# Kernel optimization log

Measured on AMD Instinct MI355X. Metric: run time of the kernel, lower is better.

## Reference

```python
import jax, jax.numpy as jnp
import numpy as np
from itertools import permutations
from math import factorial

N_MODES = 6
BATCH = 32768

# Clements mesh mode pairs for 6 modes: alternating odd/even layers, 15 MZIs total.
def clements_mode_list(n=6):
    pairs = []
    for layer in range(n):
        start = 0 if layer % 2 == 0 else 1
        for m in range(start, n - 1, 2):
            pairs.append((m, m + 1))
    return pairs

CLEMENTS_MODES = clements_mode_list(6)            # 15 pairs
ANSATZ_MODES = [(0, 1), (2, 3), (4, 5), (1, 2), (3, 4)] * 2  # 10 pairs (0-indexed)

IN_CONFIG = [1, 1, 1, 0, 0, 0]
OUT_CONFIGS = [list(c) for c in [
    [1,1,1,0,0,0],[1,1,0,1,0,0],[1,1,0,0,1,0],[1,1,0,0,0,1],[1,0,1,1,0,0],
    [1,0,1,0,1,0],[1,0,1,0,0,1],[1,0,0,1,1,0],[1,0,0,1,0,1],[1,0,0,0,1,1],
    [0,1,1,1,0,0],[0,1,1,0,1,0],[0,1,1,0,0,1],[0,1,0,1,1,0],[0,1,0,1,0,1],
    [0,1,0,0,1,1],[0,0,1,1,1,0],[0,0,1,1,0,1],[0,0,1,0,1,1],[0,0,0,1,1,1]]]

def _expand(config):  # occupation list -> repeated mode indices
    idx = []
    for m, c in enumerate(config):
        idx += [m] * int(c)
    return idx

IN_IDX = np.array(_expand(IN_CONFIG))                       # [3]
OUT_IDX = np.array([_expand(c) for c in OUT_CONFIGS])       # [20, 3]
N_PH = IN_IDX.shape[0]                                      # 3 photons
PERMS = list(permutations(range(N_PH)))                     # 6 perms of S_3
# boson-sampling normalization: sqrt(prod(in!) * prod(out!)) per output config (all 1 here)
NORM = np.array([np.sqrt(np.prod([factorial(int(v)) for v in IN_CONFIG]) *
                         np.prod([factorial(int(v)) for v in c])) for c in OUT_CONFIGS],
                dtype=np.float32)


def calc_unitary(modes, theta, phi):
    """Chain of MZI 2x2 rotations embedded in a 6x6 identity (Clements convention)."""
    U = jnp.eye(N_MODES, dtype=jnp.complex64)
    for k, (m, n) in enumerate(modes):
        ct = jnp.cos(theta[k]).astype(jnp.complex64)
        st = jnp.sin(theta[k]).astype(jnp.complex64)
        ep = jnp.exp(1j * phi[k].astype(jnp.complex64))
        T = jnp.eye(N_MODES, dtype=jnp.complex64)
        T = T.at[m, m].set(ep * ct).at[m, n].set(-st)
        T = T.at[n, m].set(ep * st).at[n, n].set(ct)
        U = T @ U
    return U


def permanent3(M):  # M: [..., 3, 3] complex -> [...] permanent over S_3
    acc = jnp.zeros(M.shape[:-2], dtype=M.dtype)
    for p in PERMS:
        acc = acc + M[..., 0, p[0]] * M[..., 1, p[1]] * M[..., 2, p[2]]
    return acc


def setup_inputs() -> dict:
    key = jax.random.key(0)
    ks = jax.random.split(key, 7)
    return {
        "x": jax.random.normal(ks[0], (BATCH, 12), dtype=jnp.float32),
        "params": jax.random.normal(ks[1], (30,), dtype=jnp.float32),
        "output_phase": jax.random.normal(ks[2], (6,), dtype=jnp.float32),
        "param_phi": jax.random.normal(ks[3], (4,), dtype=jnp.float32),
        "param_theta": jax.random.normal(ks[4], (4,), dtype=jnp.float32),
        "input_k": jax.random.normal(ks[5], (12,), dtype=jnp.float32),
        "input_b": jax.random.normal(ks[6], (12,), dtype=jnp.float32),
    }


def reference(x, params, output_phase, param_phi, param_theta, input_k, input_b):
    B = x.shape[0]
    # Static 6x6 interferometer: phi = params[0:15], theta = params[15:30]
    start = calc_unitary(CLEMENTS_MODES, params[15:30], params[0:15])
    start = jnp.diag(jnp.exp(1j * output_phase.astype(jnp.complex64))) @ start

    # Data-reuploading ansatz angles, [B, 10] each
    xs = x * input_k + input_b
    phi = jnp.concatenate([xs[:, 0:3], jnp.broadcast_to(param_phi[0:2], (B, 2)),
                           xs[:, 6:9], jnp.broadcast_to(param_phi[2:4], (B, 2))], axis=1)
    theta = jnp.concatenate([xs[:, 3:6], jnp.broadcast_to(param_theta[0:2], (B, 2)),
                             xs[:, 9:12], jnp.broadcast_to(param_theta[2:4], (B, 2))], axis=1)

    U_ans = jax.vmap(lambda t, p: calc_unitary(ANSATZ_MODES, t, p))(theta, phi)  # [B,6,6]
    U_final = U_ans @ start                                                      # [B,6,6]

    # Boson-sampling amplitudes: permanent of [out rows, in cols] submatrix
    sub = U_final[:, OUT_IDX[:, :, None], IN_IDX[None, None, :]]  # [B, 20, 3, 3]
    amps = permanent3(sub) / jnp.asarray(NORM)                    # [B, 20] complex

    # F.normalize(p=2, dim=1, eps=1e-12) on complex vectors
    norm = jnp.sqrt(jnp.sum(jnp.abs(amps) ** 2, axis=1, keepdims=True))
    amps = amps / jnp.maximum(norm, 1e-12)
    return jnp.abs(amps)
```

## Files before the change

kernel.cpp:

```cpp
#include <hip/hip_runtime.h>
#include <math.h>


__global__ __launch_bounds__(64) void bqnn_kernel(
    const float* __restrict__ x,
    const float* __restrict__ params,
    const float* __restrict__ output_phase,
    const float* __restrict__ param_phi,
    const float* __restrict__ param_theta,
    const float* __restrict__ input_k,
    const float* __restrict__ input_b,
    float* __restrict__ out,
    int B)
{
    __shared__ float sSre[6][3], sSim[6][3];
    __shared__ float sC[4][4];
    __shared__ float sK[12], sB[12];

    if (threadIdx.x == 0) {
        const int CM[15][2] = {{0,1},{2,3},{4,5},{1,2},{3,4},
                               {0,1},{2,3},{4,5},{1,2},{3,4},
                               {0,1},{2,3},{4,5},{1,2},{3,4}};
        float Vre[6][3], Vim[6][3];
        #pragma unroll
        for (int r = 0; r < 6; ++r)
            #pragma unroll
            for (int c = 0; c < 3; ++c) { Vre[r][c] = (r == c) ? 1.f : 0.f; Vim[r][c] = 0.f; }
        for (int k = 0; k < 15; ++k) {
            float ct, st, epr, epi;
            __sincosf(params[15 + k], &st, &ct);
            __sincosf(params[k],      &epi, &epr);
            int m = CM[k][0], n = CM[k][1];
            #pragma unroll
            for (int c = 0; c < 3; ++c) {
                float ar = Vre[m][c], ai = Vim[m][c];
                float br = Vre[n][c], bi = Vim[n][c];
                float tr = epr * ar - epi * ai;
                float ti = epr * ai + epi * ar;
                Vre[m][c] = ct * tr - st * br;
                Vim[m][c] = ct * ti - st * bi;
                Vre[n][c] = st * tr + ct * br;
                Vim[n][c] = st * ti + ct * bi;
            }
        }
        #pragma unroll
        for (int r = 0; r < 6; ++r) {
            float pr, pi;
            __sincosf(output_phase[r], &pi, &pr);
            #pragma unroll
            for (int c = 0; c < 3; ++c) {
                sSre[r][c] = pr * Vre[r][c] - pi * Vim[r][c];
                sSim[r][c] = pr * Vim[r][c] + pi * Vre[r][c];
            }
        }
        #pragma unroll
        for (int j = 0; j < 4; ++j) {
            float ct, st, epr, epi;
            __sincosf(param_theta[j], &st, &ct);
            __sincosf(param_phi[j],   &epi, &epr);
            sC[j][0] = ct; sC[j][1] = st; sC[j][2] = epr; sC[j][3] = epi;
        }
        #pragma unroll
        for (int i = 0; i < 12; ++i) { sK[i] = input_k[i]; sB[i] = input_b[i]; }
    }
    __syncthreads();

    int b = blockIdx.x * blockDim.x + threadIdx.x;
    if (b >= B) return;

    const float4* xp = reinterpret_cast<const float4*>(x + (size_t)b * 12);
    float4 a0 = xp[0], a1 = xp[1], a2 = xp[2];
    float xs[12] = {a0.x, a0.y, a0.z, a0.w, a1.x, a1.y, a1.z, a1.w, a2.x, a2.y, a2.z, a2.w};
    #pragma unroll
    for (int i = 0; i < 12; ++i) xs[i] = xs[i] * sK[i] + sB[i];

    float ct[10], st[10], epr[10], epi[10];
    __sincosf(xs[3],  &st[0], &ct[0]);  __sincosf(xs[0], &epi[0], &epr[0]);
    __sincosf(xs[4],  &st[1], &ct[1]);  __sincosf(xs[1], &epi[1], &epr[1]);
    __sincosf(xs[5],  &st[2], &ct[2]);  __sincosf(xs[2], &epi[2], &epr[2]);
    ct[3] = sC[0][0]; st[3] = sC[0][1]; epr[3] = sC[0][2]; epi[3] = sC[0][3];
    ct[4] = sC[1][0]; st[4] = sC[1][1]; epr[4] = sC[1][2]; epi[4] = sC[1][3];
    __sincosf(xs[9],  &st[5], &ct[5]);  __sincosf(xs[6], &epi[5], &epr[5]);
    __sincosf(xs[10], &st[6], &ct[6]);  __sincosf(xs[7], &epi[6], &epr[6]);
    __sincosf(xs[11], &st[7], &ct[7]);  __sincosf(xs[8], &epi[7], &epr[7]);
    ct[8] = sC[2][0]; st[8] = sC[2][1]; epr[8] = sC[2][2]; epi[8] = sC[2][3];
    ct[9] = sC[3][0]; st[9] = sC[3][1]; epr[9] = sC[3][2]; epi[9] = sC[3][3];

    float Vre[6][3], Vim[6][3];
    #pragma unroll
    for (int r = 0; r < 6; ++r)
        #pragma unroll
        for (int c = 0; c < 3; ++c) { Vre[r][c] = sSre[r][c]; Vim[r][c] = sSim[r][c]; }

    const int AM[10][2] = {{0,1},{2,3},{4,5},{1,2},{3,4},{0,1},{2,3},{4,5},{1,2},{3,4}};
    #pragma unroll
    for (int k = 0; k < 10; ++k) {
        int m = AM[k][0], n = AM[k][1];
        #pragma unroll
        for (int c = 0; c < 3; ++c) {
            float ar = Vre[m][c], ai = Vim[m][c];
            float br = Vre[n][c], bi = Vim[n][c];
            float tr = epr[k] * ar - epi[k] * ai;
            float ti = epr[k] * ai + epi[k] * ar;
            Vre[m][c] = ct[k] * tr - st[k] * br;
            Vim[m][c] = ct[k] * ti - st[k] * bi;
            Vre[n][c] = st[k] * tr + ct[k] * br;
            Vim[n][c] = st[k] * ti + ct[k] * bi;
        }
    }

    const int PR[10][2] = {{1,2},{1,3},{1,4},{1,5},{2,3},{2,4},{2,5},{3,4},{3,5},{4,5}};
    float q01r[10], q01i[10], q02r[10], q02i[10], q12r[10], q12i[10];
    #pragma unroll
    for (int p = 0; p < 10; ++p) {
        int i = PR[p][0], j = PR[p][1];
        q01r[p] = (Vre[i][0]*Vre[j][1] - Vim[i][0]*Vim[j][1]) + (Vre[i][1]*Vre[j][0] - Vim[i][1]*Vim[j][0]);
        q01i[p] = (Vre[i][0]*Vim[j][1] + Vim[i][0]*Vre[j][1]) + (Vre[i][1]*Vim[j][0] + Vim[i][1]*Vre[j][0]);
        q02r[p] = (Vre[i][0]*Vre[j][2] - Vim[i][0]*Vim[j][2]) + (Vre[i][2]*Vre[j][0] - Vim[i][2]*Vim[j][0]);
        q02i[p] = (Vre[i][0]*Vim[j][2] + Vim[i][0]*Vre[j][2]) + (Vre[i][2]*Vim[j][0] + Vim[i][2]*Vre[j][0]);
        q12r[p] = (Vre[i][1]*Vre[j][2] - Vim[i][1]*Vim[j][2]) + (Vre[i][2]*Vre[j][1] - Vim[i][2]*Vim[j][1]);
        q12i[p] = (Vre[i][1]*Vim[j][2] + Vim[i][1]*Vre[j][2]) + (Vre[i][2]*Vim[j][1] + Vim[i][2]*Vre[j][1]);
    }

    const int TA[20] = {0,0,0,0,0,0,0,0,0,0, 1,1,1,1,1,1, 2,2,2, 3};
    const int TP[20] = {0,1,2,3,4,5,6,7,8,9, 4,5,6,7,8,9, 7,8,9, 9};
    float sq[20];
    float ssum = 0.f;
    #pragma unroll
    for (int t = 0; t < 20; ++t) {
        int a = TA[t], p = TP[t];
        float pr = (Vre[a][0]*q12r[p] - Vim[a][0]*q12i[p])
                 + (Vre[a][1]*q02r[p] - Vim[a][1]*q02i[p])
                 + (Vre[a][2]*q01r[p] - Vim[a][2]*q01i[p]);
        float pi = (Vre[a][0]*q12i[p] + Vim[a][0]*q12r[p])
                 + (Vre[a][1]*q02i[p] + Vim[a][1]*q02r[p])
                 + (Vre[a][2]*q01i[p] + Vim[a][2]*q01r[p]);
        sq[t] = pr * pr + pi * pi;
        ssum += sq[t];
    }
    float inv = 1.f / fmaxf(sqrtf(ssum), 1e-12f);
    float res[20];
    #pragma unroll
    for (int t = 0; t < 20; ++t) res[t] = sqrtf(sq[t]) * inv;

    float4* op = reinterpret_cast<float4*>(out + (size_t)b * 20);
    op[0] = make_float4(res[0],  res[1],  res[2],  res[3]);
    op[1] = make_float4(res[4],  res[5],  res[6],  res[7]);
    op[2] = make_float4(res[8],  res[9],  res[10], res[11]);
    op[3] = make_float4(res[12], res[13], res[14], res[15]);
    op[4] = make_float4(res[16], res[17], res[18], res[19]);
}

extern "C" void kernel_launch(void* const* d_in, const int* in_sizes, int n_in,
                              void* d_out, int out_size, void* d_ws, size_t ws_size,
                              hipStream_t stream) {
    const float* x            = (const float*)d_in[0];
    const float* params       = (const float*)d_in[1];
    const float* output_phase = (const float*)d_in[2];
    const float* param_phi    = (const float*)d_in[3];
    const float* param_theta  = (const float*)d_in[4];
    const float* input_k      = (const float*)d_in[5];
    const float* input_b      = (const float*)d_in[6];
    int B = in_sizes[0] / 12;

    int block = 64;
    int grid = (B + block - 1) / block;
    bqnn_kernel<<<grid, block, 0, stream>>>(x, params, output_phase, param_phi,
                                            param_theta, input_k, input_b,
                                            (float*)d_out, B);
}
```

Baseline: 12.62 us.

## Split each batch row's permanent computation across four threads

Assigns four threads per batch element. Each thread redundantly builds the full 6x3 unitary, then computes 5 of the 20 permanents with no shared pair products. The norm is reduced across the four lanes with xor shuffles and an rsqrt. This raises parallelism and lowers per-thread register pressure, but repeats the sincos and MZI chain four times, loses the reuse of the pair products, and replaces float4 output stores with scalar stores.

```diff
diff --git a/kernel.cpp b/kernel.cpp
--- a/kernel.cpp
+++ b/kernel.cpp
@@ -2,7 +2,7 @@
 #include <math.h>
 
 
-__global__ __launch_bounds__(64) void bqnn_kernel(
+__global__ __launch_bounds__(256) void bqnn_kernel(
     const float* __restrict__ x,
     const float* __restrict__ params,
     const float* __restrict__ output_phase,
@@ -65,7 +65,9 @@
     }
     __syncthreads();
 
-    int b = blockIdx.x * blockDim.x + threadIdx.x;
+    int tid = blockIdx.x * blockDim.x + threadIdx.x;
+    int b   = tid >> 2;
+    int sub = tid & 3;
     if (b >= B) return;
 
     const float4* xp = reinterpret_cast<const float4*>(x + (size_t)b * 12);
@@ -109,46 +111,42 @@
         }
     }
 
+    const int TA[20] = {0,0,0,0,0,0,0,0,0,0, 1,1,1,1,1,1, 2,2,2, 3};
+    const int TP[20] = {0,1,2,3,4,5,6,7,8,9, 4,5,6,7,8,9, 7,8,9, 9};
     const int PR[10][2] = {{1,2},{1,3},{1,4},{1,5},{2,3},{2,4},{2,5},{3,4},{3,5},{4,5}};
-    float q01r[10], q01i[10], q02r[10], q02i[10], q12r[10], q12i[10];
+
+    float sq[5];
+    float ssum = 0.f;
     #pragma unroll
-    for (int p = 0; p < 10; ++p) {
-        int i = PR[p][0], j = PR[p][1];
-        q01r[p] = (Vre[i][0]*Vre[j][1] - Vim[i][0]*Vim[j][1]) + (Vre[i][1]*Vre[j][0] - Vim[i][1]*Vim[j][0]);
-        q01i[p] = (Vre[i][0]*Vim[j][1] + Vim[i][0]*Vre[j][1]) + (Vre[i][1]*Vim[j][0] + Vim[i][1]*Vre[j][0]);
-        q02r[p] = (Vre[i][0]*Vre[j][2] - Vim[i][0]*Vim[j][2]) + (Vre[i][2]*Vre[j][0] - Vim[i][2]*Vim[j][0]);
-        q02i[p] = (Vre[i][0]*Vim[j][2] + Vim[i][0]*Vre[j][2]) + (Vre[i][2]*Vim[j][0] + Vim[i][2]*Vre[j][0]);
-        q12r[p] = (Vre[i][1]*Vre[j][2] - Vim[i][1]*Vim[j][2]) + (Vre[i][2]*Vre[j][1] - Vim[i][2]*Vim[j][1]);
-        q12i[p] = (Vre[i][1]*Vim[j][2] + Vim[i][1]*Vre[j][2]) + (Vre[i][2]*Vim[j][1] + Vim[i][2]*Vre[j][1]);
+    for (int u = 0; u < 5; ++u) {
+        int t = 5 * sub + u;
+        int a = TA[t];
+        int i = PR[TP[t]][0], j = PR[TP[t]][1];
+
+        float q01r = (Vre[i][0]*Vre[j][1] - Vim[i][0]*Vim[j][1]) + (Vre[i][1]*Vre[j][0] - Vim[i][1]*Vim[j][0]);
+        float q01i = (Vre[i][0]*Vim[j][1] + Vim[i][0]*Vre[j][1]) + (Vre[i][1]*Vim[j][0] + Vim[i][1]*Vre[j][0]);
+        float q02r = (Vre[i][0]*Vre[j][2] - Vim[i][0]*Vim[j][2]) + (Vre[i][2]*Vre[j][0] - Vim[i][2]*Vim[j][0]);
+        float q02i = (Vre[i][0]*Vim[j][2] + Vim[i][0]*Vre[j][2]) + (Vre[i][2]*Vim[j][0] + Vim[i][2]*Vre[j][0]);
+        float q12r = (Vre[i][1]*Vre[j][2] - Vim[i][1]*Vim[j][2]) + (Vre[i][2]*Vre[j][1] - Vim[i][2]*Vim[j][1]);
+        float q12i = (Vre[i][1]*Vim[j][2] + Vim[i][1]*Vre[j][2]) + (Vre[i][2]*Vim[j][1] + Vim[i][2]*Vre[j][1]);
+
+        float pr = (Vre[a][0]*q12r - Vim[a][0]*q12i)
+                 + (Vre[a][1]*q02r - Vim[a][1]*q02i)
+                 + (Vre[a][2]*q01r - Vim[a][2]*q01i);
+        float pi = (Vre[a][0]*q12i + Vim[a][0]*q12r)
+                 + (Vre[a][1]*q02i + Vim[a][1]*q02r)
+                 + (Vre[a][2]*q01i + Vim[a][2]*q01r);
+        sq[u] = pr * pr + pi * pi;
+        ssum += sq[u];
     }
 
-    const int TA[20] = {0,0,0,0,0,0,0,0,0,0, 1,1,1,1,1,1, 2,2,2, 3};
-    const int TP[20] = {0,1,2,3,4,5,6,7,8,9, 4,5,6,7,8,9, 7,8,9, 9};
-    float sq[20];
-    float ssum = 0.f;
+    ssum += __shfl_xor(ssum, 1, 64);
+    ssum += __shfl_xor(ssum, 2, 64);
+    float inv = rsqrtf(fmaxf(ssum, 1e-24f));
+
+    float* op = out + (size_t)b * 20 + sub * 5;
     #pragma unroll
-    for (int t = 0; t < 20; ++t) {
-        int a = TA[t], p = TP[t];
-        float pr = (Vre[a][0]*q12r[p] - Vim[a][0]*q12i[p])
-                 + (Vre[a][1]*q02r[p] - Vim[a][1]*q02i[p])
-                 + (Vre[a][2]*q01r[p] - Vim[a][2]*q01i[p]);
-        float pi = (Vre[a][0]*q12i[p] + Vim[a][0]*q12r[p])
-                 + (Vre[a][1]*q02i[p] + Vim[a][1]*q02r[p])
-                 + (Vre[a][2]*q01i[p] + Vim[a][2]*q01r[p]);
-        sq[t] = pr * pr + pi * pi;
-        ssum += sq[t];
-    }
-    float inv = 1.f / fmaxf(sqrtf(ssum), 1e-12f);
-    float res[20];
-    #pragma unroll
-    for (int t = 0; t < 20; ++t) res[t] = sqrtf(sq[t]) * inv;
-
-    float4* op = reinterpret_cast<float4*>(out + (size_t)b * 20);
-    op[0] = make_float4(res[0],  res[1],  res[2],  res[3]);
-    op[1] = make_float4(res[4],  res[5],  res[6],  res[7]);
-    op[2] = make_float4(res[8],  res[9],  res[10], res[11]);
-    op[3] = make_float4(res[12], res[13], res[14], res[15]);
-    op[4] = make_float4(res[16], res[17], res[18], res[19]);
+    for (int u = 0; u < 5; ++u) op[u] = sqrtf(sq[u]) * inv;
 }
 
 extern "C" void kernel_launch(void* const* d_in, const int* in_sizes, int n_in,
@@ -163,8 +161,9 @@
     const float* input_b      = (const float*)d_in[6];
     int B = in_sizes[0] / 12;
 
-    int block = 64;
-    int grid = (B + block - 1) / block;
+    int block = 256;
+    long long threads = (long long)B * 4;
+    int grid = (int)((threads + block - 1) / block);
     bqnn_kernel<<<grid, block, 0, stream>>>(x, params, output_phase, param_phi,
                                             param_theta, input_k, input_b,
                                             (float*)d_out, B);
```

Result: slower. 20.26 us (+60.5%).

## Hoist batch-invariant unitary setup into a separate single-thread kernel

Applied to the files above, without the earlier changes.

The fixed Clements unitary, the constant ansatz rotation coefficients and the input scale/bias are now computed once by a one-thread setup kernel and written to workspace. Previously thread 0 of every block redid this work, leaving the other threads waiting at a barrier. The main kernel now reads the values straight from global memory, with no shared memory and no __syncthreads. This adds a second kernel launch and a dependency between the two kernels. The normalisation also switches to rsqrtf.

```diff
diff --git a/kernel.cpp b/kernel.cpp
--- a/kernel.cpp
+++ b/kernel.cpp
@@ -2,77 +2,91 @@
 #include <math.h>
 
 
-__global__ __launch_bounds__(64) void bqnn_kernel(
-    const float* __restrict__ x,
+__global__ void setup_kernel(
     const float* __restrict__ params,
     const float* __restrict__ output_phase,
     const float* __restrict__ param_phi,
     const float* __restrict__ param_theta,
     const float* __restrict__ input_k,
     const float* __restrict__ input_b,
+    float* __restrict__ ws)
+{
+    float pct[15], pst[15], per[15], pei[15];
+    #pragma unroll
+    for (int k = 0; k < 15; ++k) {
+        __sincosf(params[15 + k], &pst[k], &pct[k]);
+        __sincosf(params[k],      &pei[k], &per[k]);
+    }
+    const int CM[15][2] = {{0,1},{2,3},{4,5},{1,2},{3,4},
+                           {0,1},{2,3},{4,5},{1,2},{3,4},
+                           {0,1},{2,3},{4,5},{1,2},{3,4}};
+    float Vre[6][3], Vim[6][3];
+    #pragma unroll
+    for (int r = 0; r < 6; ++r)
+        #pragma unroll
+        for (int c = 0; c < 3; ++c) { Vre[r][c] = (r == c) ? 1.f : 0.f; Vim[r][c] = 0.f; }
+    #pragma unroll
+    for (int k = 0; k < 15; ++k) {
+        int m = CM[k][0], n = CM[k][1];
+        #pragma unroll
+        for (int c = 0; c < 3; ++c) {
+            float ar = Vre[m][c], ai = Vim[m][c];
+            float br = Vre[n][c], bi = Vim[n][c];
+            float tr = per[k] * ar - pei[k] * ai;
+            float ti = per[k] * ai + pei[k] * ar;
+            Vre[m][c] = pct[k] * tr - pst[k] * br;
+            Vim[m][c] = pct[k] * ti - pst[k] * bi;
+            Vre[n][c] = pst[k] * tr + pct[k] * br;
+            Vim[n][c] = pst[k] * ti + pct[k] * bi;
+        }
+    }
+    #pragma unroll
+    for (int r = 0; r < 6; ++r) {
+        float pr, pi;
+        __sincosf(output_phase[r], &pi, &pr);
+        #pragma unroll
+        for (int c = 0; c < 3; ++c) {
+            ws[r * 3 + c]      = pr * Vre[r][c] - pi * Vim[r][c];
+            ws[18 + r * 3 + c] = pr * Vim[r][c] + pi * Vre[r][c];
+        }
+    }
+    #pragma unroll
+    for (int j = 0; j < 4; ++j) {
+        float ct, st, epr, epi;
+        __sincosf(param_theta[j], &st, &ct);
+        __sincosf(param_phi[j],   &epi, &epr);
+        ws[36 + j * 4 + 0] = ct;  ws[36 + j * 4 + 1] = st;
+        ws[36 + j * 4 + 2] = epr; ws[36 + j * 4 + 3] = epi;
+    }
+    #pragma unroll
+    for (int i = 0; i < 12; ++i) { ws[52 + i] = input_k[i]; ws[64 + i] = input_b[i]; }
+}
+
+__global__ __launch_bounds__(64) void bqnn_kernel(
+    const float* __restrict__ x,
+    const float* __restrict__ ws,
     float* __restrict__ out,
     int B)
 {
-    __shared__ float sSre[6][3], sSim[6][3];
-    __shared__ float sC[4][4];
-    __shared__ float sK[12], sB[12];
-
-    if (threadIdx.x == 0) {
-        const int CM[15][2] = {{0,1},{2,3},{4,5},{1,2},{3,4},
-                               {0,1},{2,3},{4,5},{1,2},{3,4},
-                               {0,1},{2,3},{4,5},{1,2},{3,4}};
-        float Vre[6][3], Vim[6][3];
-        #pragma unroll
-        for (int r = 0; r < 6; ++r)
-            #pragma unroll
-            for (int c = 0; c < 3; ++c) { Vre[r][c] = (r == c) ? 1.f : 0.f; Vim[r][c] = 0.f; }
-        for (int k = 0; k < 15; ++k) {
-            float ct, st, epr, epi;
-            __sincosf(params[15 + k], &st, &ct);
-            __sincosf(params[k],      &epi, &epr);
-            int m = CM[k][0], n = CM[k][1];
-            #pragma unroll
-            for (int c = 0; c < 3; ++c) {
-                float ar = Vre[m][c], ai = Vim[m][c];
-                float br = Vre[n][c], bi = Vim[n][c];
-                float tr = epr * ar - epi * ai;
-                float ti = epr * ai + epi * ar;
-                Vre[m][c] = ct * tr - st * br;
-                Vim[m][c] = ct * ti - st * bi;
-                Vre[n][c] = st * tr + ct * br;
-                Vim[n][c] = st * ti + ct * bi;
-            }
-        }
-        #pragma unroll
-        for (int r = 0; r < 6; ++r) {
-            float pr, pi;
-            __sincosf(output_phase[r], &pi, &pr);
-            #pragma unroll
-            for (int c = 0; c < 3; ++c) {
-                sSre[r][c] = pr * Vre[r][c] - pi * Vim[r][c];
-                sSim[r][c] = pr * Vim[r][c] + pi * Vre[r][c];
-            }
-        }
-        #pragma unroll
-        for (int j = 0; j < 4; ++j) {
-            float ct, st, epr, epi;
-            __sincosf(param_theta[j], &st, &ct);
-            __sincosf(param_phi[j],   &epi, &epr);
-            sC[j][0] = ct; sC[j][1] = st; sC[j][2] = epr; sC[j][3] = epi;
-        }
-        #pragma unroll
-        for (int i = 0; i < 12; ++i) { sK[i] = input_k[i]; sB[i] = input_b[i]; }
-    }
-    __syncthreads();
-
     int b = blockIdx.x * blockDim.x + threadIdx.x;
     if (b >= B) return;
+
+    float Sre[6][3], Sim[6][3];
+    #pragma unroll
+    for (int r = 0; r < 6; ++r)
+        #pragma unroll
+        for (int c = 0; c < 3; ++c) { Sre[r][c] = ws[r * 3 + c]; Sim[r][c] = ws[18 + r * 3 + c]; }
+    float sC[4][4];
+    #pragma unroll
+    for (int j = 0; j < 4; ++j)
+        #pragma unroll
+        for (int q = 0; q < 4; ++q) sC[j][q] = ws[36 + j * 4 + q];
 
     const float4* xp = reinterpret_cast<const float4*>(x + (size_t)b * 12);
     float4 a0 = xp[0], a1 = xp[1], a2 = xp[2];
     float xs[12] = {a0.x, a0.y, a0.z, a0.w, a1.x, a1.y, a1.z, a1.w, a2.x, a2.y, a2.z, a2.w};
     #pragma unroll
-    for (int i = 0; i < 12; ++i) xs[i] = xs[i] * sK[i] + sB[i];
+    for (int i = 0; i < 12; ++i) xs[i] = xs[i] * ws[52 + i] + ws[64 + i];
 
     float ct[10], st[10], epr[10], epi[10];
     __sincosf(xs[3],  &st[0], &ct[0]);  __sincosf(xs[0], &epi[0], &epr[0]);
@@ -90,7 +104,7 @@
     #pragma unroll
     for (int r = 0; r < 6; ++r)
         #pragma unroll
-        for (int c = 0; c < 3; ++c) { Vre[r][c] = sSre[r][c]; Vim[r][c] = sSim[r][c]; }
+        for (int c = 0; c < 3; ++c) { Vre[r][c] = Sre[r][c]; Vim[r][c] = Sim[r][c]; }
 
     const int AM[10][2] = {{0,1},{2,3},{4,5},{1,2},{3,4},{0,1},{2,3},{4,5},{1,2},{3,4}};
     #pragma unroll
@@ -138,7 +152,7 @@
         sq[t] = pr * pr + pi * pi;
         ssum += sq[t];
     }
-    float inv = 1.f / fmaxf(sqrtf(ssum), 1e-12f);
+    float inv = rsqrtf(fmaxf(ssum, 1e-24f));
     float res[20];
     #pragma unroll
     for (int t = 0; t < 20; ++t) res[t] = sqrtf(sq[t]) * inv;
@@ -162,10 +176,12 @@
     const float* input_k      = (const float*)d_in[5];
     const float* input_b      = (const float*)d_in[6];
     int B = in_sizes[0] / 12;
+    float* ws = (float*)d_ws;
+
+    setup_kernel<<<1, 1, 0, stream>>>(params, output_phase, param_phi, param_theta,
+                                      input_k, input_b, ws);
 
     int block = 64;
     int grid = (B + block - 1) / block;
-    bqnn_kernel<<<grid, block, 0, stream>>>(x, params, output_phase, param_phi,
-                                            param_theta, input_k, input_b,
-                                            (float*)d_out, B);
+    bqnn_kernel<<<grid, block, 0, stream>>>(x, ws, (float*)d_out, B);
 }
```

After: 15.17 us. 1.2x slower.

## Process two batch elements per thread and parallelize constant-mesh setup across lanes

Applied to the files above, without the earlier changes.

Each thread now handles two batch elements (tid and tid+half), and the grid is halved. The serial thread-0 setup is replaced: 44 lanes compute the sincos values in parallel, and every thread then rebuilds the fixed 6x3 mesh product in registers, which removes the long single-lane prologue before the barrier. The q-products and permanent evaluation are fused into a single loop. The gains are more ILP per thread and a shorter serialized prologue. In exchange, register pressure goes up, and every thread redoes the mesh setup.

```diff
diff --git a/kernel.cpp b/kernel.cpp
--- a/kernel.cpp
+++ b/kernel.cpp
@@ -13,142 +13,163 @@
     float* __restrict__ out,
     int B)
 {
-    __shared__ float sSre[6][3], sSim[6][3];
-    __shared__ float sC[4][4];
-    __shared__ float sK[12], sB[12];
+    __shared__ float sc[88];
+    int lane = threadIdx.x;
+    if (lane < 44) {
+        float arg;
+        if      (lane < 15) arg = params[15 + lane];
+        else if (lane < 30) arg = params[lane - 15];
+        else if (lane < 36) arg = output_phase[lane - 30];
+        else if (lane < 40) arg = param_theta[lane - 36];
+        else                arg = param_phi[lane - 40];
+        float s, c;
+        __sincosf(arg, &s, &c);
+        sc[2 * lane]     = s;
+        sc[2 * lane + 1] = c;
+    }
+    __syncthreads();
 
-    if (threadIdx.x == 0) {
-        const int CM[15][2] = {{0,1},{2,3},{4,5},{1,2},{3,4},
-                               {0,1},{2,3},{4,5},{1,2},{3,4},
-                               {0,1},{2,3},{4,5},{1,2},{3,4}};
-        float Vre[6][3], Vim[6][3];
+    const int CM[15][2] = {{0,1},{2,3},{4,5},{1,2},{3,4},
+                           {0,1},{2,3},{4,5},{1,2},{3,4},
+                           {0,1},{2,3},{4,5},{1,2},{3,4}};
+    float Sre[6][3], Sim[6][3];
+    #pragma unroll
+    for (int r = 0; r < 6; ++r)
+        #pragma unroll
+        for (int c = 0; c < 3; ++c) { Sre[r][c] = (r == c) ? 1.f : 0.f; Sim[r][c] = 0.f; }
+    #pragma unroll
+    for (int k = 0; k < 15; ++k) {
+        float pst = sc[2 * k],        pct = sc[2 * k + 1];
+        float pei = sc[2 * (15 + k)], per = sc[2 * (15 + k) + 1];
+        int m = CM[k][0], n = CM[k][1];
+        #pragma unroll
+        for (int c = 0; c < 3; ++c) {
+            float ar = Sre[m][c], ai = Sim[m][c];
+            float br = Sre[n][c], bi = Sim[n][c];
+            float tr = per * ar - pei * ai;
+            float ti = per * ai + pei * ar;
+            Sre[m][c] = pct * tr - pst * br;
+            Sim[m][c] = pct * ti - pst * bi;
+            Sre[n][c] = pst * tr + pct * br;
+            Sim[n][c] = pst * ti + pct * bi;
+        }
+    }
+    #pragma unroll
+    for (int r = 0; r < 6; ++r) {
+        float pi = sc[2 * (30 + r)], pr = sc[2 * (30 + r) + 1];
+        #pragma unroll
+        for (int c = 0; c < 3; ++c) {
+            float vr = Sre[r][c], vi = Sim[r][c];
+            Sre[r][c] = pr * vr - pi * vi;
+            Sim[r][c] = pr * vi + pi * vr;
+        }
+    }
+
+    int half = (B + 1) >> 1;
+    int tid = blockIdx.x * blockDim.x + threadIdx.x;
+    if (tid >= half) return;
+    int e1v = tid + half;
+    bool has1 = (e1v < B);
+    int eidx[2] = { tid, has1 ? e1v : tid };
+
+    float xs[2][12];
+    #pragma unroll
+    for (int e = 0; e < 2; ++e) {
+        const float4* xp = reinterpret_cast<const float4*>(x + (size_t)eidx[e] * 12);
+        float4 a0 = xp[0], a1 = xp[1], a2 = xp[2];
+        float t[12] = {a0.x, a0.y, a0.z, a0.w, a1.x, a1.y, a1.z, a1.w, a2.x, a2.y, a2.z, a2.w};
+        #pragma unroll
+        for (int i = 0; i < 12; ++i) xs[e][i] = t[i] * input_k[i] + input_b[i];
+    }
+
+    float ct[2][10], st[2][10], epr[2][10], epi[2][10];
+    #pragma unroll
+    for (int e = 0; e < 2; ++e) {
+        __sincosf(xs[e][3],  &st[e][0], &ct[e][0]);  __sincosf(xs[e][0], &epi[e][0], &epr[e][0]);
+        __sincosf(xs[e][4],  &st[e][1], &ct[e][1]);  __sincosf(xs[e][1], &epi[e][1], &epr[e][1]);
+        __sincosf(xs[e][5],  &st[e][2], &ct[e][2]);  __sincosf(xs[e][2], &epi[e][2], &epr[e][2]);
+        st[e][3] = sc[2*36]; ct[e][3] = sc[2*36+1];  epi[e][3] = sc[2*40]; epr[e][3] = sc[2*40+1];
+        st[e][4] = sc[2*37]; ct[e][4] = sc[2*37+1];  epi[e][4] = sc[2*41]; epr[e][4] = sc[2*41+1];
+        __sincosf(xs[e][9],  &st[e][5], &ct[e][5]);  __sincosf(xs[e][6], &epi[e][5], &epr[e][5]);
+        __sincosf(xs[e][10], &st[e][6], &ct[e][6]);  __sincosf(xs[e][7], &epi[e][6], &epr[e][6]);
+        __sincosf(xs[e][11], &st[e][7], &ct[e][7]);  __sincosf(xs[e][8], &epi[e][7], &epr[e][7]);
+        st[e][8] = sc[2*38]; ct[e][8] = sc[2*38+1];  epi[e][8] = sc[2*42]; epr[e][8] = sc[2*42+1];
+        st[e][9] = sc[2*39]; ct[e][9] = sc[2*39+1];  epi[e][9] = sc[2*43]; epr[e][9] = sc[2*43+1];
+    }
+
+    float Vre[2][6][3], Vim[2][6][3];
+    #pragma unroll
+    for (int e = 0; e < 2; ++e)
         #pragma unroll
         for (int r = 0; r < 6; ++r)
             #pragma unroll
-            for (int c = 0; c < 3; ++c) { Vre[r][c] = (r == c) ? 1.f : 0.f; Vim[r][c] = 0.f; }
-        for (int k = 0; k < 15; ++k) {
-            float ct, st, epr, epi;
-            __sincosf(params[15 + k], &st, &ct);
-            __sincosf(params[k],      &epi, &epr);
-            int m = CM[k][0], n = CM[k][1];
-            #pragma unroll
-            for (int c = 0; c < 3; ++c) {
-                float ar = Vre[m][c], ai = Vim[m][c];
-                float br = Vre[n][c], bi = Vim[n][c];
-                float tr = epr * ar - epi * ai;
-                float ti = epr * ai + epi * ar;
-                Vre[m][c] = ct * tr - st * br;
-                Vim[m][c] = ct * ti - st * bi;
-                Vre[n][c] = st * tr + ct * br;
-                Vim[n][c] = st * ti + ct * bi;
-            }
-        }
-        #pragma unroll
-        for (int r = 0; r < 6; ++r) {
-            float pr, pi;
-            __sincosf(output_phase[r], &pi, &pr);
-            #pragma unroll
-            for (int c = 0; c < 3; ++c) {
-                sSre[r][c] = pr * Vre[r][c] - pi * Vim[r][c];
-                sSim[r][c] = pr * Vim[r][c] + pi * Vre[r][c];
-            }
-        }
-        #pragma unroll
-        for (int j = 0; j < 4; ++j) {
-            float ct, st, epr, epi;
-            __sincosf(param_theta[j], &st, &ct);
-            __sincosf(param_phi[j],   &epi, &epr);
-            sC[j][0] = ct; sC[j][1] = st; sC[j][2] = epr; sC[j][3] = epi;
-        }
-        #pragma unroll
-        for (int i = 0; i < 12; ++i) { sK[i] = input_k[i]; sB[i] = input_b[i]; }
-    }
-    __syncthreads();
-
-    int b = blockIdx.x * blockDim.x + threadIdx.x;
-    if (b >= B) return;
-
-    const float4* xp = reinterpret_cast<const float4*>(x + (size_t)b * 12);
-    float4 a0 = xp[0], a1 = xp[1], a2 = xp[2];
-    float xs[12] = {a0.x, a0.y, a0.z, a0.w, a1.x, a1.y, a1.z, a1.w, a2.x, a2.y, a2.z, a2.w};
-    #pragma unroll
-    for (int i = 0; i < 12; ++i) xs[i] = xs[i] * sK[i] + sB[i];
-
-    float ct[10], st[10], epr[10], epi[10];
-    __sincosf(xs[3],  &st[0], &ct[0]);  __sincosf(xs[0], &epi[0], &epr[0]);
-    __sincosf(xs[4],  &st[1], &ct[1]);  __sincosf(xs[1], &epi[1], &epr[1]);
-    __sincosf(xs[5],  &st[2], &ct[2]);  __sincosf(xs[2], &epi[2], &epr[2]);
-    ct[3] = sC[0][0]; st[3] = sC[0][1]; epr[3] = sC[0][2]; epi[3] = sC[0][3];
-    ct[4] = sC[1][0]; st[4] = sC[1][1]; epr[4] = sC[1][2]; epi[4] = sC[1][3];
-    __sincosf(xs[9],  &st[5], &ct[5]);  __sincosf(xs[6], &epi[5], &epr[5]);
-    __sincosf(xs[10], &st[6], &ct[6]);  __sincosf(xs[7], &epi[6], &epr[6]);
-    __sincosf(xs[11], &st[7], &ct[7]);  __sincosf(xs[8], &epi[7], &epr[7]);
-    ct[8] = sC[2][0]; st[8] = sC[2][1]; epr[8] = sC[2][2]; epi[8] = sC[2][3];
-    ct[9] = sC[3][0]; st[9] = sC[3][1]; epr[9] = sC[3][2]; epi[9] = sC[3][3];
-
-    float Vre[6][3], Vim[6][3];
-    #pragma unroll
-    for (int r = 0; r < 6; ++r)
-        #pragma unroll
-        for (int c = 0; c < 3; ++c) { Vre[r][c] = sSre[r][c]; Vim[r][c] = sSim[r][c]; }
+            for (int c = 0; c < 3; ++c) { Vre[e][r][c] = Sre[r][c]; Vim[e][r][c] = Sim[r][c]; }
 
     const int AM[10][2] = {{0,1},{2,3},{4,5},{1,2},{3,4},{0,1},{2,3},{4,5},{1,2},{3,4}};
     #pragma unroll
     for (int k = 0; k < 10; ++k) {
         int m = AM[k][0], n = AM[k][1];
         #pragma unroll
-        for (int c = 0; c < 3; ++c) {
-            float ar = Vre[m][c], ai = Vim[m][c];
-            float br = Vre[n][c], bi = Vim[n][c];
-            float tr = epr[k] * ar - epi[k] * ai;
-            float ti = epr[k] * ai + epi[k] * ar;
-            Vre[m][c] = ct[k] * tr - st[k] * br;
-            Vim[m][c] = ct[k] * ti - st[k] * bi;
-            Vre[n][c] = st[k] * tr + ct[k] * br;
-            Vim[n][c] = st[k] * ti + ct[k] * bi;
+        for (int e = 0; e < 2; ++e) {
+            #pragma unroll
+            for (int c = 0; c < 3; ++c) {
+                float ar = Vre[e][m][c], ai = Vim[e][m][c];
+                float br = Vre[e][n][c], bi = Vim[e][n][c];
+                float tr = epr[e][k] * ar - epi[e][k] * ai;
+                float ti = epr[e][k] * ai + epi[e][k] * ar;
+                Vre[e][m][c] = ct[e][k] * tr - st[e][k] * br;
+                Vim[e][m][c] = ct[e][k] * ti - st[e][k] * bi;
+                Vre[e][n][c] = st[e][k] * tr + ct[e][k] * br;
+                Vim[e][n][c] = st[e][k] * ti + ct[e][k] * bi;
+            }
         }
     }
 
     const int PR[10][2] = {{1,2},{1,3},{1,4},{1,5},{2,3},{2,4},{2,5},{3,4},{3,5},{4,5}};
-    float q01r[10], q01i[10], q02r[10], q02i[10], q12r[10], q12i[10];
+    float sq[2][20];
+    float ssum[2] = {0.f, 0.f};
     #pragma unroll
     for (int p = 0; p < 10; ++p) {
         int i = PR[p][0], j = PR[p][1];
-        q01r[p] = (Vre[i][0]*Vre[j][1] - Vim[i][0]*Vim[j][1]) + (Vre[i][1]*Vre[j][0] - Vim[i][1]*Vim[j][0]);
-        q01i[p] = (Vre[i][0]*Vim[j][1] + Vim[i][0]*Vre[j][1]) + (Vre[i][1]*Vim[j][0] + Vim[i][1]*Vre[j][0]);
-        q02r[p] = (Vre[i][0]*Vre[j][2] - Vim[i][0]*Vim[j][2]) + (Vre[i][2]*Vre[j][0] - Vim[i][2]*Vim[j][0]);
-        q02i[p] = (Vre[i][0]*Vim[j][2] + Vim[i][0]*Vre[j][2]) + (Vre[i][2]*Vim[j][0] + Vim[i][2]*Vre[j][0]);
-        q12r[p] = (Vre[i][1]*Vre[j][2] - Vim[i][1]*Vim[j][2]) + (Vre[i][2]*Vre[j][1] - Vim[i][2]*Vim[j][1]);
-        q12i[p] = (Vre[i][1]*Vim[j][2] + Vim[i][1]*Vre[j][2]) + (Vre[i][2]*Vim[j][1] + Vim[i][2]*Vre[j][1]);
+        #pragma unroll
+        for (int e = 0; e < 2; ++e) {
+            float q01r = (Vre[e][i][0]*Vre[e][j][1] - Vim[e][i][0]*Vim[e][j][1]) + (Vre[e][i][1]*Vre[e][j][0] - Vim[e][i][1]*Vim[e][j][0]);
+            float q01i = (Vre[e][i][0]*Vim[e][j][1] + Vim[e][i][0]*Vre[e][j][1]) + (Vre[e][i][1]*Vim[e][j][0] + Vim[e][i][1]*Vre[e][j][0]);
+            float q02r = (Vre[e][i][0]*Vre[e][j][2] - Vim[e][i][0]*Vim[e][j][2]) + (Vre[e][i][2]*Vre[e][j][0] - Vim[e][i][2]*Vim[e][j][0]);
+            float q02i = (Vre[e][i][0]*Vim[e][j][2] + Vim[e][i][0]*Vre[e][j][2]) + (Vre[e][i][2]*Vim[e][j][0] + Vim[e][i][2]*Vre[e][j][0]);
+            float q12r = (Vre[e][i][1]*Vre[e][j][2] - Vim[e][i][1]*Vim[e][j][2]) + (Vre[e][i][2]*Vre[e][j][1] - Vim[e][i][2]*Vim[e][j][1]);
+            float q12i = (Vre[e][i][1]*Vim[e][j][2] + Vim[e][i][1]*Vre[e][j][2]) + (Vre[e][i][2]*Vim[e][j][1] + Vim[e][i][2]*Vre[e][j][1]);
+            #pragma unroll
+            for (int a = 0; a < 4; ++a) {
+                if ((a == 0) || (a == 1 && p >= 4) || (a == 2 && p >= 7) || (a == 3 && p == 9)) {
+                    int t = (a == 0) ? p : (a == 1) ? 10 + (p - 4) : (a == 2) ? 16 + (p - 7) : 19;
+                    float pr = (Vre[e][a][0]*q12r - Vim[e][a][0]*q12i)
+                             + (Vre[e][a][1]*q02r - Vim[e][a][1]*q02i)
+                             + (Vre[e][a][2]*q01r - Vim[e][a][2]*q01i);
+                    float pi = (Vre[e][a][0]*q12i + Vim[e][a][0]*q12r)
+                             + (Vre[e][a][1]*q02i + Vim[e][a][1]*q02r)
+                             + (Vre[e][a][2]*q01i + Vim[e][a][2]*q01r);
+                    sq[e][t] = pr * pr + pi * pi;
+                    ssum[e] += sq[e][t];
+                }
+            }
+        }
     }
 
-    const int TA[20] = {0,0,0,0,0,0,0,0,0,0, 1,1,1,1,1,1, 2,2,2, 3};
-    const int TP[20] = {0,1,2,3,4,5,6,7,8,9, 4,5,6,7,8,9, 7,8,9, 9};
-    float sq[20];
-    float ssum = 0.f;
     #pragma unroll
-    for (int t = 0; t < 20; ++t) {
-        int a = TA[t], p = TP[t];
-        float pr = (Vre[a][0]*q12r[p] - Vim[a][0]*q12i[p])
-                 + (Vre[a][1]*q02r[p] - Vim[a][1]*q02i[p])
-                 + (Vre[a][2]*q01r[p] - Vim[a][2]*q01i[p]);
-        float pi = (Vre[a][0]*q12i[p] + Vim[a][0]*q12r[p])
-                 + (Vre[a][1]*q02i[p] + Vim[a][1]*q02r[p])
-                 + (Vre[a][2]*q01i[p] + Vim[a][2]*q01r[p]);
-        sq[t] = pr * pr + pi * pi;
-        ssum += sq[t];
+    for (int e = 0; e < 2; ++e) {
+        if (e == 1 && !has1) break;
+        float inv = rsqrtf(fmaxf(ssum[e], 1e-24f));
+        float res[20];
+        #pragma unroll
+        for (int t = 0; t < 20; ++t) res[t] = sqrtf(sq[e][t]) * inv;
+        float4* op = reinterpret_cast<float4*>(out + (size_t)eidx[e] * 20);
+        op[0] = make_float4(res[0],  res[1],  res[2],  res[3]);
+        op[1] = make_float4(res[4],  res[5],  res[6],  res[7]);
+        op[2] = make_float4(res[8],  res[9],  res[10], res[11]);
+        op[3] = make_float4(res[12], res[13], res[14], res[15]);
+        op[4] = make_float4(res[16], res[17], res[18], res[19]);
     }
-    float inv = 1.f / fmaxf(sqrtf(ssum), 1e-12f);
-    float res[20];
-    #pragma unroll
-    for (int t = 0; t < 20; ++t) res[t] = sqrtf(sq[t]) * inv;
-
-    float4* op = reinterpret_cast<float4*>(out + (size_t)b * 20);
-    op[0] = make_float4(res[0],  res[1],  res[2],  res[3]);
-    op[1] = make_float4(res[4],  res[5],  res[6],  res[7]);
-    op[2] = make_float4(res[8],  res[9],  res[10], res[11]);
-    op[3] = make_float4(res[12], res[13], res[14], res[15]);
-    op[4] = make_float4(res[16], res[17], res[18], res[19]);
 }
 
 extern "C" void kernel_launch(void* const* d_in, const int* in_sizes, int n_in,
@@ -163,8 +184,9 @@
     const float* input_b      = (const float*)d_in[6];
     int B = in_sizes[0] / 12;
 
+    int half = (B + 1) / 2;
     int block = 64;
-    int grid = (B + block - 1) / block;
+    int grid = (half + block - 1) / block;
     bqnn_kernel<<<grid, block, 0, stream>>>(x, params, output_phase, param_phi,
                                             param_theta, input_k, input_b,
                                             (float*)d_out, B);
```

Measured after the change: 14.29 us. 13.2% more time.
